# Kernel tuning notes

Measured on AMD Instinct MI355X. Metric: run time of the kernel, lower is better.

Reference implementation:

```python
import jax, jax.numpy as jnp
import numpy as np

L, H, C, V, T_MAX = 12, 12, 768, 50257, 1024
D = C // H
LN_EPS = 1e-5


def layer_norm(x, w, b):
    m = jnp.mean(x, axis=-1, keepdims=True)
    v = jnp.mean(jnp.square(x - m), axis=-1, keepdims=True)
    return (x - m) * jax.lax.rsqrt(v + LN_EPS) * w + b


def setup_inputs() -> dict:
    key = jax.random.key(0)
    ks = jax.random.split(key, 16)
    B, T = 2, 1024
    s = 0.02
    inp = {
        "idx": jax.random.randint(ks[0], (B, T), 0, V),
        "wte": jax.random.normal(ks[1], (V, C), jnp.float32) * s,
        "wpe": jax.random.normal(ks[2], (T_MAX, C), jnp.float32) * s,
        # stacked per-layer params, leading axis = layer
        "ln1_w": jnp.ones((L, C), jnp.float32),
        "ln1_b": jnp.zeros((L, C), jnp.float32),
        "Wq": jax.random.normal(ks[3], (L, C, C), jnp.float32) * s,
        "bq": jnp.zeros((L, C), jnp.float32),
        "Wk": jax.random.normal(ks[4], (L, C, C), jnp.float32) * s,
        "bk": jnp.zeros((L, C), jnp.float32),
        "Wv": jax.random.normal(ks[5], (L, C, C), jnp.float32) * s,
        "bv": jnp.zeros((L, C), jnp.float32),
        "Wo": jax.random.normal(ks[6], (L, C, C), jnp.float32) * (s / np.sqrt(2 * L)),
        "bo": jnp.zeros((L, C), jnp.float32),
        "ln2_w": jnp.ones((L, C), jnp.float32),
        "ln2_b": jnp.zeros((L, C), jnp.float32),
        "Wfc": jax.random.normal(ks[7], (L, C, 4 * C), jnp.float32) * s,
        "bfc": jnp.zeros((L, 4 * C), jnp.float32),
        "Wpr": jax.random.normal(ks[8], (L, 4 * C, C), jnp.float32) * (s / np.sqrt(2 * L)),
        "bpr": jnp.zeros((L, C), jnp.float32),
        "ln_f_w": jnp.ones((C,), jnp.float32),
        "ln_f_b": jnp.zeros((C,), jnp.float32),
        "Wlm": jax.random.normal(ks[9], (C, V), jnp.float32) * s,
    }
    return inp


def _forward(idx, wte, wpe, ln1_w, ln1_b, Wq, bq, Wk, bk, Wv, bv, Wo, bo,
             ln2_w, ln2_b, Wfc, bfc, Wpr, bpr, ln_f_w, ln_f_b, Wlm):
    B, T = idx.shape
    x = wte[idx] + wpe[jnp.arange(T)][None, :, :]  # (B,T,C)
    causal = jnp.tril(jnp.ones((T, T), bool))  # (T,T) causal mask
    scale = 1.0 / np.sqrt(D)
    neg_inf = jnp.finfo(x.dtype).min

    def block(x, p):
        (l1w, l1b, wq, bq_, wk, bk_, wv, bv_, wo, bo_,
         l2w, l2b, wfc, bfc_, wpr, bpr_) = p
        h = layer_norm(x, l1w, l1b)
        q = (h @ wq + bq_).reshape(B, T, H, D)
        k = (h @ wk + bk_).reshape(B, T, H, D)
        v = (h @ wv + bv_).reshape(B, T, H, D)
        scores = jnp.einsum("bqhd,bkhd->bhqk", q, k) * scale
        scores = jnp.where(causal[None, None], scores, neg_inf)
        attn = jax.nn.softmax(scores, axis=-1)
        y = jnp.einsum("bhqk,bkhd->bqhd", attn, v).reshape(B, T, C)
        x = x + y @ wo + bo_
        h2 = layer_norm(x, l2w, l2b)
        x = x + jax.nn.gelu(h2 @ wfc + bfc_, approximate=False) @ wpr + bpr_
        return x, None

    params = (ln1_w, ln1_b, Wq, bq, Wk, bk, Wv, bv, Wo, bo,
              ln2_w, ln2_b, Wfc, bfc, Wpr, bpr)
    x, _ = jax.lax.scan(block, x, params)
    x = layer_norm(x, ln_f_w, ln_f_b)
    logits = x @ Wlm  # (B,T,V)
    return logits


def reference(idx, wte, wpe, ln1_w, ln1_b, Wq, bq, Wk, bk, Wv, bv, Wo, bo,
              ln2_w, ln2_b, Wfc, bfc, Wpr, bpr, ln_f_w, ln_f_b, Wlm):
    return _forward(idx, wte, wpe, ln1_w, ln1_b, Wq, bq, Wk, bk, Wv, bv, Wo, bo,
                    ln2_w, ln2_b, Wfc, bfc, Wpr, bpr, ln_f_w, ln_f_b, Wlm)
```

## Files before the change

### kernel.cpp

```cpp
#include <hip/hip_runtime.h>
#include <math.h>
#include <cstddef>


#define Cdim 768
#define Hn   12
#define Ln   12
#define Tn   1024
#define Bn   2
#define Mrows (Bn * Tn)

typedef unsigned short ushort_t;
typedef __bf16 bf16x8 __attribute__((ext_vector_type(8)));
typedef float  f32x4  __attribute__((ext_vector_type(4)));

__device__ __forceinline__ ushort_t f2bf(float v) {
    union { float f; unsigned int u; } x; x.f = v;
    unsigned int r = x.u + 0x7fffu + ((x.u >> 16) & 1u);
    return (ushort_t)(r >> 16);
}
__device__ __forceinline__ float gelu_f(float v) {
    return 0.5f * v * (1.0f + erff(v * 0.70710678118654752f));
}
__device__ __forceinline__ void gload16(const void* g, void* l) {
    __builtin_amdgcn_global_load_lds(
        (const __attribute__((address_space(1))) unsigned int*)g,
        (__attribute__((address_space(3))) unsigned int*)l, 16, 0, 0);
}

__global__ void embed_k(const int* __restrict__ idx, const float* __restrict__ wte,
                        const float* __restrict__ wpe, float* __restrict__ x) {
    int i = blockIdx.x * 256 + threadIdx.x;
    int c  = i % Cdim;
    int bt = i / Cdim;
    int t  = bt % Tn;
    int tok = idx[bt];
    x[i] = wte[(size_t)tok * Cdim + c] + wpe[(size_t)t * Cdim + c];
}

__global__ __launch_bounds__(256) void ln_k(const float* __restrict__ x,
                                            const float* __restrict__ w,
                                            const float* __restrict__ b,
                                            ushort_t* __restrict__ out) {
    int row = blockIdx.x;
    const float* xr = x + (size_t)row * Cdim;
    int t = threadIdx.x;
    float v0 = xr[t], v1 = xr[t + 256], v2 = xr[t + 512];
    float s = v0 + v1 + v2;
    #pragma unroll
    for (int o = 32; o > 0; o >>= 1) s += __shfl_xor(s, o);
    __shared__ float red[8];
    int wid = t >> 6;
    if ((t & 63) == 0) red[wid] = s;
    __syncthreads();
    float mean = (red[0] + red[1] + red[2] + red[3]) * (1.0f / 768.0f);
    float d0 = v0 - mean, d1 = v1 - mean, d2 = v2 - mean;
    float sq = d0 * d0 + d1 * d1 + d2 * d2;
    #pragma unroll
    for (int o = 32; o > 0; o >>= 1) sq += __shfl_xor(sq, o);
    if ((t & 63) == 0) red[4 + wid] = sq;
    __syncthreads();
    float var = (red[4] + red[5] + red[6] + red[7]) * (1.0f / 768.0f);
    float rstd = rsqrtf(var + 1e-5f);
    ushort_t* orow = out + (size_t)row * Cdim;
    orow[t]       = f2bf(d0 * rstd * w[t]       + b[t]);
    orow[t + 256] = f2bf(d1 * rstd * w[t + 256] + b[t + 256]);
    orow[t + 512] = f2bf(d2 * rstd * w[t + 512] + b[t + 512]);
}

__device__ __forceinline__ void tconv_tile(const float* __restrict__ W,
                                           ushort_t* __restrict__ WT,
                                           int K, int N, int n0, int k0, bool guard) {
    __shared__ float t[32][33];
    int x = threadIdx.x & 31, y = threadIdx.x >> 5;
    #pragma unroll
    for (int j = 0; j < 4; ++j) {
        int kk = k0 + y + j * 8, nn = n0 + x;
        t[y + j * 8][x] = (!guard || nn < N) ? W[(size_t)kk * N + nn] : 0.0f;
    }
    __syncthreads();
    #pragma unroll
    for (int j = 0; j < 4; ++j) {
        int nn = n0 + y + j * 8, kk = k0 + x;
        WT[(size_t)nn * K + kk] = f2bf(t[x][y + j * 8]);
    }
}

__global__ __launch_bounds__(256) void wconv_k(const float* __restrict__ W,
                                               ushort_t* __restrict__ WT,
                                               int K, int N) {
    tconv_tile(W, WT, K, N, blockIdx.x * 32, blockIdx.y * 32, true);
}

__device__ __forceinline__ void conv_body(
    int bid,
    const float* Wq, const float* Wk, const float* Wv, const float* Wo,
    const float* Wfc, const float* Wpr,
    const float* bq, const float* bk, const float* bv,
    ushort_t* wqkvt, ushort_t* wot, ushort_t* wfct, ushort_t* wprt,
    float* bqkv) {
    if (bid < 2304) {
        int z = bid / 576, t = bid % 576;
        const float* W = (z == 0) ? Wq : (z == 1) ? Wk : (z == 2) ? Wv : Wo;
        ushort_t* dst = (z < 3) ? (wqkvt + (size_t)z * 768 * 768) : wot;
        tconv_tile(W, dst, 768, 768, (t % 24) * 32, (t / 24) * 32, false);
    } else if (bid < 4608) {
        int t = bid - 2304;
        tconv_tile(Wfc, wfct, 768, 3072, (t % 96) * 32, (t / 96) * 32, false);
    } else if (bid < 6912) {
        int t = bid - 4608;
        tconv_tile(Wpr, wprt, 3072, 768, (t % 24) * 32, (t / 24) * 32, false);
    } else {
        int i = (bid - 6912) * 256 + threadIdx.x;
        bqkv[i] = (i < 768) ? bq[i] : (i < 1536 ? bk[i - 768] : bv[i - 1536]);
    }
}

__global__ __launch_bounds__(256) void conv_layer_k(
    const float* Wq, const float* Wk, const float* Wv, const float* Wo,
    const float* Wfc, const float* Wpr,
    const float* bq, const float* bk, const float* bv,
    ushort_t* wqkvt, ushort_t* wot, ushort_t* wfct, ushort_t* wprt,
    float* bqkv) {
    conv_body(blockIdx.x, Wq, Wk, Wv, Wo, Wfc, Wpr, bq, bk, bv,
              wqkvt, wot, wfct, wprt, bqkv);
}

__global__ __launch_bounds__(256) void conv_all_k(
    const float* Wq, const float* Wk, const float* Wv, const float* Wo,
    const float* Wfc, const float* Wpr,
    const float* bq, const float* bk, const float* bv,
    ushort_t* wqkvt, ushort_t* wot, ushort_t* wfct, ushort_t* wprt,
    float* bqkv) {
    int l = blockIdx.x / 6921, bid = blockIdx.x % 6921;
    const size_t o2 = (size_t)l * 768 * 768;
    const size_t o4 = (size_t)l * 768 * 3072;
    conv_body(bid,
              Wq + o2, Wk + o2, Wv + o2, Wo + o2, Wfc + o4, Wpr + o4,
              bq + l * 768, bk + l * 768, bv + l * 768,
              wqkvt + (size_t)l * 2304 * 768, wot + o2,
              wfct + o4, wprt + o4, bqkv + l * 2304);
}

template <int BM, int BN, int TH, int WGN,
          bool BIAS, bool GELU_, bool RES, bool OUTBF16, bool XCD, bool QKV>
__global__ __launch_bounds__(TH, 2) void gemm_pipe_k(
    const ushort_t* __restrict__ A,
    const ushort_t* __restrict__ Bt,
    const float* __restrict__ bias,
    const float* __restrict__ res,
    void* __restrict__ Cout,
    ushort_t* __restrict__ kdst,
    ushort_t* __restrict__ vdst,
    int M, int N, int K, int cpx, int mtiles) {
    constexpr int SA = BM * 128;
    constexpr int SB = BN * 128;
    constexpr int WM = BM / 2;
    constexpr int WN = BN / WGN;
    constexpr int FM = WM / 16;
    constexpr int FN = WN / 16;
    constexpr int RJ = TH / 8;
    constexpr int JA = BM / RJ;
    constexpr int JB = BN / RJ;
    constexpr int NL = JA + JB;
    static_assert(NL == 4 || NL == 6 || NL == 8, "vmcnt immediate");
    __shared__ char lds[2 * (SA + SB)];
    char* Abase = lds;
    char* Bbase = lds + 2 * SA;

    const int tid = threadIdx.x;
    const int lane = tid & 63;
    const int w = tid >> 6;
    const int wr = w / WGN, wc = w % WGN;
    int m0, n0;
    if (XCD) {
        int lid = ((int)blockIdx.x & 7) * cpx + ((int)blockIdx.x >> 3);
        m0 = (lid % mtiles) * BM;
        n0 = (lid / mtiles) * BN;
    } else {
        m0 = blockIdx.y * BM;
        n0 = blockIdx.x * BN;
    }

    f32x4 acc[FM][FN] = {};

    const int srowl = tid >> 3;
    const int sslot = (tid & 7) ^ (srowl & 7);
    const ushort_t* Asrc = A  + (size_t)(m0 + srowl) * K + sslot * 8;
    const ushort_t* Bsrc = Bt + (size_t)(n0 + srowl) * K + sslot * 8;

    auto stageall = [&](int d, int kt) {
        const ushort_t* As = Asrc + kt * 64;
        const ushort_t* Bs = Bsrc + kt * 64;
        #pragma unroll
        for (int j = 0; j < JA; ++j)
            gload16(As + (size_t)(j * RJ) * K, Abase + d * SA + tid * 16 + j * (TH * 16));
        #pragma unroll
        for (int j = 0; j < JB; ++j)
            gload16(Bs + (size_t)(j * RJ) * K, Bbase + d * SB + tid * 16 + j * (TH * 16));
    };
    auto readA = [&](int d, int m, int ks) -> bf16x8 {
        int rl = wr * WM + m * 16 + (lane & 15);
        int s  = ks * 4 + (lane >> 4);
        return *(const bf16x8*)(Abase + d * SA + rl * 128 + ((s ^ (rl & 7)) << 4));
    };
    auto readB = [&](int d, int n, int ks) -> bf16x8 {
        int rl = wc * WN + n * 16 + (lane & 15);
        int s  = ks * 4 + (lane >> 4);
        return *(const bf16x8*)(Bbase + d * SB + rl * 128 + ((s ^ (rl & 7)) << 4));
    };

    const int nt = K >> 6;
    stageall(0, 0);
    for (int kt = 0; kt < nt; ++kt) {
        const int d = kt & 1;
        if (kt + 1 < nt) {
            stageall(d ^ 1, kt + 1);
            if constexpr (NL == 8)      asm volatile("s_waitcnt vmcnt(8)" ::: "memory");
            else if constexpr (NL == 6) asm volatile("s_waitcnt vmcnt(6)" ::: "memory");
            else                        asm volatile("s_waitcnt vmcnt(4)" ::: "memory");
        } else {
            asm volatile("s_waitcnt vmcnt(0)" ::: "memory");
        }
        __builtin_amdgcn_s_barrier();
        asm volatile("" ::: "memory");

        bf16x8 bfr[FN][2];
        #pragma unroll
        for (int n = 0; n < FN; ++n) {
            bfr[n][0] = readB(d, n, 0);
            bfr[n][1] = readB(d, n, 1);
        }
        __builtin_amdgcn_s_setprio(1);
        #pragma unroll
        for (int m = 0; m < FM; ++m) {
            bf16x8 a0 = readA(d, m, 0);
            bf16x8 a1 = readA(d, m, 1);
            #pragma unroll
            for (int n = 0; n < FN; ++n) {
                acc[m][n] = __builtin_amdgcn_mfma_f32_16x16x32_bf16(
                    a0, bfr[n][0], acc[m][n], 0, 0, 0);
                acc[m][n] = __builtin_amdgcn_mfma_f32_16x16x32_bf16(
                    a1, bfr[n][1], acc[m][n], 0, 0, 0);
            }
        }
        __builtin_amdgcn_s_setprio(0);
        asm volatile("" ::: "memory");
        __builtin_amdgcn_s_barrier();
    }

    const int r0 = (lane >> 4) * 4, c0 = lane & 15;
    if constexpr (QKV) {
        const int region = n0 / 768;
        #pragma unroll
        for (int m = 0; m < FM; ++m)
            #pragma unroll
            for (int n = 0; n < FN; ++n) {
                int col = n0 + wc * WN + n * 16 + c0;
                int row0 = m0 + wr * WM + m * 16 + r0;
                float vv[4];
                #pragma unroll
                for (int q = 0; q < 4; ++q) vv[q] = acc[m][n][q] + bias[col];
                if (region == 0) {
                    #pragma unroll
                    for (int q = 0; q < 4; ++q)
                        ((ushort_t*)Cout)[(size_t)(row0 + q) * 768 + col] = f2bf(vv[q]);
                } else if (region == 1) {
                    int ck = col - 768, h = ck >> 6, dd = ck & 63;
                    #pragma unroll
                    for (int q = 0; q < 4; ++q) {
                        int row = row0 + q;
                        kdst[(((size_t)(row >> 10) * Hn + h) * Tn + (row & 1023)) * 64 + dd]
                            = f2bf(vv[q]);
                    }
                } else {
                    int cv = col - 1536, h = cv >> 6, dd = cv & 63;
                    int bb = row0 >> 10, tok = row0 & 1023;
                    ushort4 pk;
                    pk.x = f2bf(vv[0]); pk.y = f2bf(vv[1]);
                    pk.z = f2bf(vv[2]); pk.w = f2bf(vv[3]);
                    *(ushort4*)&vdst[(((size_t)bb * Hn + h) * 64 + dd) * Tn + tok] = pk;
                }
            }
        return;
    }
    #pragma unroll
    for (int m = 0; m < FM; ++m)
        #pragma unroll
        for (int n = 0; n < FN; ++n) {
            int col = n0 + wc * WN + n * 16 + c0;
            if (col < N) {
                #pragma unroll
                for (int q = 0; q < 4; ++q) {
                    int row = m0 + wr * WM + m * 16 + r0 + q;
                    float v = acc[m][n][q];
                    if (BIAS) v += bias[col];
                    if (GELU_) v = gelu_f(v);
                    if (RES) v += res[(size_t)row * N + col];
                    if (OUTBF16) ((ushort_t*)Cout)[(size_t)row * N + col] = f2bf(v);
                    else         ((float*)Cout)[(size_t)row * N + col] = v;
                }
            }
        }
}

__global__ __launch_bounds__(256) void attn_mfma_k(
    const ushort_t* __restrict__ qb,
    const ushort_t* __restrict__ kpb,
    const ushort_t* __restrict__ vtb,
    ushort_t* __restrict__ yb) {
    __shared__ ushort_t Ks[64][72];
    __shared__ ushort_t Vt[64][72];
    __shared__ ushort_t Pl[4][16][72];
    const int chunk = (Tn / 64 - 1) - blockIdx.x;
    const int h = blockIdx.y, b = blockIdx.z;
    const int tid = threadIdx.x, lane = tid & 63, w = tid >> 6;
    const int c = lane & 15, g = lane >> 4;
    const int qrow0 = chunk * 64 + w * 16;

    const ushort_t* qp = qb + (size_t)(b * Tn + qrow0 + c) * Cdim + h * 64 + g * 8;
    bf16x8 qa0 = *(const bf16x8*)qp;
    bf16x8 qa1 = *(const bf16x8*)(qp + 32);

    f32x4 accO[4] = {};
    float mrun[4], lrun[4];
    #pragma unroll
    for (int q = 0; q < 4; ++q) { mrun[q] = -1e30f; lrun[q] = 0.0f; }

    const int skey = tid >> 2, sd0 = (tid & 3) * 16;
    const ushort_t* ksrc = kpb + ((size_t)(b * Hn + h) * Tn + skey) * 64 + sd0;
    const int vd = tid >> 2, vseg = tid & 3;
    const ushort_t* vsrc = vtb + ((size_t)(b * Hn + h) * 64 + vd) * Tn + vseg * 16;
    ushort_t* KsW = &Ks[skey][sd0];
    ushort_t* VtW = &Vt[vd][vseg * 16];

    uint4 kr0, kr1, vr0, vr1;
    auto loadt = [&](int kt) {
        const ushort_t* kp = ksrc + (size_t)kt * 64 * 64;
        kr0 = *(const uint4*)kp;
        kr1 = *(const uint4*)(kp + 8);
        const ushort_t* vp = vsrc + kt * 64;
        vr0 = *(const uint4*)vp;
        vr1 = *(const uint4*)(vp + 8);
    };

    const int ntiles = chunk + 1;
    loadt(0);
    for (int kt = 0; kt < ntiles; ++kt) {
        __syncthreads();
        *(uint4*)KsW       = kr0;
        *(uint4*)(KsW + 8) = kr1;
        *(uint4*)VtW       = vr0;
        *(uint4*)(VtW + 8) = vr1;
        __syncthreads();
        if (kt + 1 < ntiles) loadt(kt + 1);

        f32x4 sf[4];
        #pragma unroll
        for (int nk = 0; nk < 4; ++nk) {
            bf16x8 kf0 = *(const bf16x8*)&Ks[nk * 16 + c][g * 8];
            bf16x8 kf1 = *(const bf16x8*)&Ks[nk * 16 + c][g * 8 + 32];
            f32x4 z = {};
            z = __builtin_amdgcn_mfma_f32_16x16x32_bf16(qa0, kf0, z, 0, 0, 0);
            z = __builtin_amdgcn_mfma_f32_16x16x32_bf16(qa1, kf1, z, 0, 0, 0);
            sf[nk] = z;
        }
        float pmax[4] = {-1e30f, -1e30f, -1e30f, -1e30f};
        #pragma unroll
        for (int nk = 0; nk < 4; ++nk) {
            int key = kt * 64 + nk * 16 + c;
            #pragma unroll
            for (int q = 0; q < 4; ++q) {
                float sv = sf[nk][q];
                int row = qrow0 + g * 4 + q;
                sv = (key > row) ? -1e30f : sv;
                sf[nk][q] = sv;
                pmax[q] = fmaxf(pmax[q], sv);
            }
        }
        #pragma unroll
        for (int q = 0; q < 4; ++q)
            #pragma unroll
            for (int off = 1; off < 16; off <<= 1)
                pmax[q] = fmaxf(pmax[q], __shfl_xor(pmax[q], off));
        float corr[4], psum[4];
        #pragma unroll
        for (int q = 0; q < 4; ++q) {
            float mn = fmaxf(mrun[q], pmax[q]);
            corr[q] = __expf((mrun[q] - mn) * 0.125f);
            mrun[q] = mn;
            psum[q] = 0.0f;
        }
        #pragma unroll
        for (int nk = 0; nk < 4; ++nk)
            #pragma unroll
            for (int q = 0; q < 4; ++q) {
                float p = __expf((sf[nk][q] - mrun[q]) * 0.125f);
                psum[q] += p;
                Pl[w][g * 4 + q][nk * 16 + c] = f2bf(p);
            }
        #pragma unroll
        for (int q = 0; q < 4; ++q) {
            #pragma unroll
            for (int off = 1; off < 16; off <<= 1)
                psum[q] += __shfl_xor(psum[q], off);
            lrun[q] = lrun[q] * corr[q] + psum[q];
        }
        #pragma unroll
        for (int ni = 0; ni < 4; ++ni)
            #pragma unroll
            for (int q = 0; q < 4; ++q)
                accO[ni][q] *= corr[q];

        asm volatile("" ::: "memory");
        bf16x8 pa0 = *(const bf16x8*)&Pl[w][c][g * 8];
        bf16x8 pa1 = *(const bf16x8*)&Pl[w][c][g * 8 + 32];
        #pragma unroll
        for (int ni = 0; ni < 4; ++ni) {
            bf16x8 bv0 = *(const bf16x8*)&Vt[ni * 16 + c][g * 8];
            bf16x8 bv1 = *(const bf16x8*)&Vt[ni * 16 + c][g * 8 + 32];
            accO[ni] = __builtin_amdgcn_mfma_f32_16x16x32_bf16(pa0, bv0, accO[ni], 0, 0, 0);
            accO[ni] = __builtin_amdgcn_mfma_f32_16x16x32_bf16(pa1, bv1, accO[ni], 0, 0, 0);
        }
    }

    #pragma unroll
    for (int q = 0; q < 4; ++q) {
        float inv = 1.0f / lrun[q];
        ushort_t* yr = yb + (size_t)(b * Tn + qrow0 + g * 4 + q) * Cdim + h * 64;
        #pragma unroll
        for (int ni = 0; ni < 4; ++ni)
            yr[ni * 16 + c] = f2bf(accO[ni][q] * inv);
    }
}

extern "C" void kernel_launch(void* const* d_in, const int* in_sizes, int n_in,
                              void* d_out, int out_size, void* d_ws, size_t ws_size,
                              hipStream_t stream) {
    const int*   idx  = (const int*)d_in[0];
    const float* wte  = (const float*)d_in[1];
    const float* wpe  = (const float*)d_in[2];
    const float* ln1w = (const float*)d_in[3];
    const float* ln1b = (const float*)d_in[4];
    const float* Wq   = (const float*)d_in[5];
    const float* bq   = (const float*)d_in[6];
    const float* Wk   = (const float*)d_in[7];
    const float* bk   = (const float*)d_in[8];
    const float* Wv   = (const float*)d_in[9];
    const float* bv   = (const float*)d_in[10];
    const float* Wo   = (const float*)d_in[11];
    const float* bo   = (const float*)d_in[12];
    const float* ln2w = (const float*)d_in[13];
    const float* ln2b = (const float*)d_in[14];
    const float* Wfc  = (const float*)d_in[15];
    const float* bfc  = (const float*)d_in[16];
    const float* Wpr  = (const float*)d_in[17];
    const float* bpr  = (const float*)d_in[18];
    const float* lnfw = (const float*)d_in[19];
    const float* lnfb = (const float*)d_in[20];
    const float* Wlm  = (const float*)d_in[21];
    float* out = (float*)d_out;

    const int M = Mrows;
    const int V = out_size / M;
    const int Vpad = ((V + 255) / 256) * 256;

    const size_t SZ_QKV = (size_t)2304 * 768;
    const size_t SZ_O   = (size_t)768 * 768;
    const size_t SZ_FC  = (size_t)3072 * 768;
    const size_t SZ_PR  = (size_t)768 * 3072;
    const size_t SZ_L   = SZ_QKV + SZ_O + SZ_FC + SZ_PR;

    float*    x     = (float*)d_ws;
    float*    bqkvb = x + (size_t)M * Cdim;
    ushort_t* qb    = (ushort_t*)(bqkvb + 12 * 2304);
    ushort_t* kpb   = qb + (size_t)M * Cdim;
    ushort_t* vtb   = kpb + (size_t)Bn * Hn * Tn * 64;
    ushort_t* hb    = vtb + (size_t)Bn * Hn * 64 * Tn;
    ushort_t* yb    = hb + (size_t)M * Cdim;
    ushort_t* mid   = yb + (size_t)M * Cdim;
    ushort_t* wlmt  = mid + (size_t)M * 3072;
    ushort_t* wbase = wlmt + (size_t)Vpad * Cdim;

    const size_t used_common = (size_t)((char*)wbase - (char*)d_ws);
    const bool big = ws_size >= used_common + 12 * SZ_L * sizeof(ushort_t);

    embed_k<<<(M * Cdim) / 256, 256, 0, stream>>>(idx, wte, wpe, x);
    wconv_k<<<dim3(Vpad / 32, 24), 256, 0, stream>>>(Wlm, wlmt, Cdim, V);

    ushort_t* wqkvt0 = wbase;
    ushort_t* wot0   = wqkvt0 + SZ_QKV;
    ushort_t* wfct0  = wot0 + SZ_O;
    ushort_t* wprt0  = wfct0 + SZ_FC;

    if (big) {
        ushort_t* qkvt_all = wbase;
        ushort_t* ot_all   = qkvt_all + 12 * SZ_QKV;
        ushort_t* fct_all  = ot_all + 12 * SZ_O;
        ushort_t* prt_all  = fct_all + 12 * SZ_FC;
        conv_all_k<<<12 * 6921, 256, 0, stream>>>(
            Wq, Wk, Wv, Wo, Wfc, Wpr, bq, bk, bv,
            qkvt_all, ot_all, fct_all, prt_all, bqkvb);
        for (int l = 0; l < Ln; ++l) {
            ushort_t* wqkvt = qkvt_all + (size_t)l * SZ_QKV;
            ushort_t* wot   = ot_all   + (size_t)l * SZ_O;
            ushort_t* wfct  = fct_all  + (size_t)l * SZ_FC;
            ushort_t* wprt  = prt_all  + (size_t)l * SZ_PR;
            float*    bqkv  = bqkvb + l * 2304;
            ln_k<<<M, 256, 0, stream>>>(x, ln1w + l * Cdim, ln1b + l * Cdim, hb);
            gemm_pipe_k<128, 64, 256, 2, true, false, false, true, false, true>
                <<<dim3(36, 16), 256, 0, stream>>>(
                hb, wqkvt, bqkv, nullptr, qb, kpb, vtb, M, 2304, Cdim, 0, 0);
            attn_mfma_k<<<dim3(16, Hn, Bn), 256, 0, stream>>>(qb, kpb, vtb, yb);
            gemm_pipe_k<64, 64, 256, 2, true, false, true, false, false, false>
                <<<dim3(12, 32), 256, 0, stream>>>(
                yb, wot, bo + l * Cdim, x, x, nullptr, nullptr, M, Cdim, Cdim, 0, 0);
            ln_k<<<M, 256, 0, stream>>>(x, ln2w + l * Cdim, ln2b + l * Cdim, hb);
            gemm_pipe_k<128, 64, 256, 2, true, true, false, true, false, false>
                <<<dim3(48, 16), 256, 0, stream>>>(
                hb, wfct, bfc + (size_t)l * 4 * Cdim, nullptr, mid,
                nullptr, nullptr, M, 3072, Cdim, 0, 0);
            gemm_pipe_k<64, 64, 256, 2, true, false, true, false, false, false>
                <<<dim3(12, 32), 256, 0, stream>>>(
                mid, wprt, bpr + l * Cdim, x, x, nullptr, nullptr, M, Cdim, 3072, 0, 0);
        }
    } else {
        for (int l = 0; l < Ln; ++l) {
            const size_t wo2 = (size_t)l * Cdim * Cdim;
            const size_t wo4 = (size_t)l * Cdim * 4 * Cdim;
            conv_layer_k<<<6921, 256, 0, stream>>>(
                Wq + wo2, Wk + wo2, Wv + wo2, Wo + wo2, Wfc + wo4, Wpr + wo4,
                bq + l * Cdim, bk + l * Cdim, bv + l * Cdim,
                wqkvt0, wot0, wfct0, wprt0, bqkvb);
            ln_k<<<M, 256, 0, stream>>>(x, ln1w + l * Cdim, ln1b + l * Cdim, hb);
            gemm_pipe_k<128, 64, 256, 2, true, false, false, true, false, true>
                <<<dim3(36, 16), 256, 0, stream>>>(
                hb, wqkvt0, bqkvb, nullptr, qb, kpb, vtb, M, 2304, Cdim, 0, 0);
            attn_mfma_k<<<dim3(16, Hn, Bn), 256, 0, stream>>>(qb, kpb, vtb, yb);
            gemm_pipe_k<64, 64, 256, 2, true, false, true, false, false, false>
                <<<dim3(12, 32), 256, 0, stream>>>(
                yb, wot0, bo + l * Cdim, x, x, nullptr, nullptr, M, Cdim, Cdim, 0, 0);
            ln_k<<<M, 256, 0, stream>>>(x, ln2w + l * Cdim, ln2b + l * Cdim, hb);
            gemm_pipe_k<128, 64, 256, 2, true, true, false, true, false, false>
                <<<dim3(48, 16), 256, 0, stream>>>(
                hb, wfct0, bfc + (size_t)l * 4 * Cdim, nullptr, mid,
                nullptr, nullptr, M, 3072, Cdim, 0, 0);
            gemm_pipe_k<64, 64, 256, 2, true, false, true, false, false, false>
                <<<dim3(12, 32), 256, 0, stream>>>(
                mid, wprt0, bpr + l * Cdim, x, x, nullptr, nullptr, M, Cdim, 3072, 0, 0);
        }
    }

    ln_k<<<M, 256, 0, stream>>>(x, lnfw, lnfb, hb);
    const int nblk = 16 * (Vpad / 128);
    gemm_pipe_k<128, 128, 256, 2, false, false, false, false, true, false>
        <<<nblk, 256, 0, stream>>>(
        hb, wlmt, nullptr, nullptr, out, nullptr, nullptr, M, V, Cdim, nblk / 8, 16);
}
```

Baseline: 1.785 ms.

## Split-K the N=768 projection GEMMs and fold the reduction into LayerNorm

The attention-output and MLP-projection GEMMs (N=768) now run split-K with two K halves. Each half writes an fp32 partial to its own buffer. The following LayerNorm kernel sums the residual, both partials and the bias, writes the updated residual back, and then normalizes. The aim is to double block count on these under-occupied GEMMs and drop their separate residual/bias epilogue, at the cost of extra fp32 partial-buffer traffic and more loads in LayerNorm.

```diff
diff --git a/kernel.cpp b/kernel.cpp
--- a/kernel.cpp
+++ b/kernel.cpp
@@ -38,14 +38,27 @@
     x[i] = wte[(size_t)tok * Cdim + c] + wpe[(size_t)t * Cdim + c];
 }
 
-__global__ __launch_bounds__(256) void ln_k(const float* __restrict__ x,
+template <bool HASP>
+__global__ __launch_bounds__(256) void ln_k(float* __restrict__ x,
+                                            const float* __restrict__ p0,
+                                            const float* __restrict__ p1,
+                                            const float* __restrict__ pb,
                                             const float* __restrict__ w,
                                             const float* __restrict__ b,
                                             ushort_t* __restrict__ out) {
     int row = blockIdx.x;
-    const float* xr = x + (size_t)row * Cdim;
+    float* xr = x + (size_t)row * Cdim;
     int t = threadIdx.x;
-    float v0 = xr[t], v1 = xr[t + 256], v2 = xr[t + 512];
+    float v0, v1, v2;
+    if (HASP) {
+        size_t base = (size_t)row * Cdim;
+        v0 = xr[t]       + p0[base + t]       + p1[base + t]       + pb[t];
+        v1 = xr[t + 256] + p0[base + t + 256] + p1[base + t + 256] + pb[t + 256];
+        v2 = xr[t + 512] + p0[base + t + 512] + p1[base + t + 512] + pb[t + 512];
+        xr[t] = v0; xr[t + 256] = v1; xr[t + 512] = v2;
+    } else {
+        v0 = xr[t]; v1 = xr[t + 256]; v2 = xr[t + 512];
+    }
     float s = v0 + v1 + v2;
     #pragma unroll
     for (int o = 32; o > 0; o >>= 1) s += __shfl_xor(s, o);
@@ -143,7 +156,8 @@
 }
 
 template <int BM, int BN, int TH, int WGN,
-          bool BIAS, bool GELU_, bool RES, bool OUTBF16, bool XCD, bool QKV>
+          bool BIAS, bool GELU_, bool RES, bool OUTBF16, bool XCD, bool QKV,
+          bool SPLITK>
 __global__ __launch_bounds__(TH, 2) void gemm_pipe_k(
     const ushort_t* __restrict__ A,
     const ushort_t* __restrict__ Bt,
@@ -152,7 +166,7 @@
     void* __restrict__ Cout,
     ushort_t* __restrict__ kdst,
     ushort_t* __restrict__ vdst,
-    int M, int N, int K, int cpx, int mtiles) {
+    int M, int N, int K, int Kloop, int cpx, int mtiles) {
     constexpr int SA = BM * 128;
     constexpr int SB = BN * 128;
     constexpr int WM = BM / 2;
@@ -181,13 +195,15 @@
         m0 = blockIdx.y * BM;
         n0 = blockIdx.x * BN;
     }
+    const int kz = SPLITK ? (int)blockIdx.z : 0;
+    const size_t kzoff = (size_t)kz * Kloop;
 
     f32x4 acc[FM][FN] = {};
 
     const int srowl = tid >> 3;
     const int sslot = (tid & 7) ^ (srowl & 7);
-    const ushort_t* Asrc = A  + (size_t)(m0 + srowl) * K + sslot * 8;
-    const ushort_t* Bsrc = Bt + (size_t)(n0 + srowl) * K + sslot * 8;
+    const ushort_t* Asrc = A  + (size_t)(m0 + srowl) * K + kzoff + sslot * 8;
+    const ushort_t* Bsrc = Bt + (size_t)(n0 + srowl) * K + kzoff + sslot * 8;
 
     auto stageall = [&](int d, int kt) {
         const ushort_t* As = Asrc + kt * 64;
@@ -210,7 +226,7 @@
         return *(const bf16x8*)(Bbase + d * SB + rl * 128 + ((s ^ (rl & 7)) << 4));
     };
 
-    const int nt = K >> 6;
+    const int nt = Kloop >> 6;
     stageall(0, 0);
     for (int kt = 0; kt < nt; ++kt) {
         const int d = kt & 1;
@@ -284,6 +300,21 @@
             }
         return;
     }
+    if constexpr (SPLITK) {
+        float* dst = (float*)Cout + (size_t)kz * M * N;
+        #pragma unroll
+        for (int m = 0; m < FM; ++m)
+            #pragma unroll
+            for (int n = 0; n < FN; ++n) {
+                int col = n0 + wc * WN + n * 16 + c0;
+                #pragma unroll
+                for (int q = 0; q < 4; ++q) {
+                    int row = m0 + wr * WM + m * 16 + r0 + q;
+                    dst[(size_t)row * N + col] = acc[m][n][q];
+                }
+            }
+        return;
+    }
     #pragma unroll
     for (int m = 0; m < FM; ++m)
         #pragma unroll
@@ -473,7 +504,9 @@
 
     float*    x     = (float*)d_ws;
     float*    bqkvb = x + (size_t)M * Cdim;
-    ushort_t* qb    = (ushort_t*)(bqkvb + 12 * 2304);
+    float*    opart = bqkvb + 12 * 2304;
+    float*    ppart = opart + 2 * (size_t)M * Cdim;
+    ushort_t* qb    = (ushort_t*)(ppart + 2 * (size_t)M * Cdim);
     ushort_t* kpb   = qb + (size_t)M * Cdim;
     ushort_t* vtb   = kpb + (size_t)Bn * Hn * Tn * 64;
     ushort_t* hb    = vtb + (size_t)Bn * Hn * 64 * Tn;
@@ -493,67 +526,75 @@
     ushort_t* wfct0  = wot0 + SZ_O;
     ushort_t* wprt0  = wfct0 + SZ_FC;
 
-    if (big) {
-        ushort_t* qkvt_all = wbase;
-        ushort_t* ot_all   = qkvt_all + 12 * SZ_QKV;
-        ushort_t* fct_all  = ot_all + 12 * SZ_O;
-        ushort_t* prt_all  = fct_all + 12 * SZ_FC;
+    ushort_t* qkvt_all = wbase;
+    ushort_t* ot_all   = qkvt_all + 12 * SZ_QKV;
+    ushort_t* fct_all  = ot_all + 12 * SZ_O;
+    ushort_t* prt_all  = fct_all + 12 * SZ_FC;
+
+    if (big)
         conv_all_k<<<12 * 6921, 256, 0, stream>>>(
             Wq, Wk, Wv, Wo, Wfc, Wpr, bq, bk, bv,
             qkvt_all, ot_all, fct_all, prt_all, bqkvb);
-        for (int l = 0; l < Ln; ++l) {
-            ushort_t* wqkvt = qkvt_all + (size_t)l * SZ_QKV;
-            ushort_t* wot   = ot_all   + (size_t)l * SZ_O;
-            ushort_t* wfct  = fct_all  + (size_t)l * SZ_FC;
-            ushort_t* wprt  = prt_all  + (size_t)l * SZ_PR;
-            float*    bqkv  = bqkvb + l * 2304;
-            ln_k<<<M, 256, 0, stream>>>(x, ln1w + l * Cdim, ln1b + l * Cdim, hb);
-            gemm_pipe_k<128, 64, 256, 2, true, false, false, true, false, true>
-                <<<dim3(36, 16), 256, 0, stream>>>(
-                hb, wqkvt, bqkv, nullptr, qb, kpb, vtb, M, 2304, Cdim, 0, 0);
-            attn_mfma_k<<<dim3(16, Hn, Bn), 256, 0, stream>>>(qb, kpb, vtb, yb);
-            gemm_pipe_k<64, 64, 256, 2, true, false, true, false, false, false>
-                <<<dim3(12, 32), 256, 0, stream>>>(
-                yb, wot, bo + l * Cdim, x, x, nullptr, nullptr, M, Cdim, Cdim, 0, 0);
-            ln_k<<<M, 256, 0, stream>>>(x, ln2w + l * Cdim, ln2b + l * Cdim, hb);
-            gemm_pipe_k<128, 64, 256, 2, true, true, false, true, false, false>
-                <<<dim3(48, 16), 256, 0, stream>>>(
-                hb, wfct, bfc + (size_t)l * 4 * Cdim, nullptr, mid,
-                nullptr, nullptr, M, 3072, Cdim, 0, 0);
-            gemm_pipe_k<64, 64, 256, 2, true, false, true, false, false, false>
-                <<<dim3(12, 32), 256, 0, stream>>>(
-                mid, wprt, bpr + l * Cdim, x, x, nullptr, nullptr, M, Cdim, 3072, 0, 0);
-        }
-    } else {
-        for (int l = 0; l < Ln; ++l) {
+
+    for (int l = 0; l < Ln; ++l) {
+        ushort_t *wqkvt, *wot, *wfct, *wprt;
+        float* bqkv;
+        if (big) {
+            wqkvt = qkvt_all + (size_t)l * SZ_QKV;
+            wot   = ot_all   + (size_t)l * SZ_O;
+            wfct  = fct_all  + (size_t)l * SZ_FC;
+            wprt  = prt_all  + (size_t)l * SZ_PR;
+            bqkv  = bqkvb + l * 2304;
+        } else {
             const size_t wo2 = (size_t)l * Cdim * Cdim;
             const size_t wo4 = (size_t)l * Cdim * 4 * Cdim;
             conv_layer_k<<<6921, 256, 0, stream>>>(
                 Wq + wo2, Wk + wo2, Wv + wo2, Wo + wo2, Wfc + wo4, Wpr + wo4,
                 bq + l * Cdim, bk + l * Cdim, bv + l * Cdim,
                 wqkvt0, wot0, wfct0, wprt0, bqkvb);
-            ln_k<<<M, 256, 0, stream>>>(x, ln1w + l * Cdim, ln1b + l * Cdim, hb);
-            gemm_pipe_k<128, 64, 256, 2, true, false, false, true, false, true>
-                <<<dim3(36, 16), 256, 0, stream>>>(
-                hb, wqkvt0, bqkvb, nullptr, qb, kpb, vtb, M, 2304, Cdim, 0, 0);
-            attn_mfma_k<<<dim3(16, Hn, Bn), 256, 0, stream>>>(qb, kpb, vtb, yb);
-            gemm_pipe_k<64, 64, 256, 2, true, false, true, false, false, false>
-                <<<dim3(12, 32), 256, 0, stream>>>(
-                yb, wot0, bo + l * Cdim, x, x, nullptr, nullptr, M, Cdim, Cdim, 0, 0);
-            ln_k<<<M, 256, 0, stream>>>(x, ln2w + l * Cdim, ln2b + l * Cdim, hb);
-            gemm_pipe_k<128, 64, 256, 2, true, true, false, true, false, false>
-                <<<dim3(48, 16), 256, 0, stream>>>(
-                hb, wfct0, bfc + (size_t)l * 4 * Cdim, nullptr, mid,
-                nullptr, nullptr, M, 3072, Cdim, 0, 0);
-            gemm_pipe_k<64, 64, 256, 2, true, false, true, false, false, false>
-                <<<dim3(12, 32), 256, 0, stream>>>(
-                mid, wprt0, bpr + l * Cdim, x, x, nullptr, nullptr, M, Cdim, 3072, 0, 0);
-        }
-    }
-
-    ln_k<<<M, 256, 0, stream>>>(x, lnfw, lnfb, hb);
+            wqkvt = wqkvt0; wot = wot0; wfct = wfct0; wprt = wprt0; bqkv = bqkvb;
+        }
+
+        if (l == 0)
+            ln_k<false><<<M, 256, 0, stream>>>(
+                x, nullptr, nullptr, nullptr, ln1w, ln1b, hb);
+        else
+            ln_k<true><<<M, 256, 0, stream>>>(
+                x, ppart, ppart + (size_t)M * Cdim, bpr + (l - 1) * Cdim,
+                ln1w + l * Cdim, ln1b + l * Cdim, hb);
+
+        gemm_pipe_k<128, 64, 256, 2, true, false, false, true, false, true, false>
+            <<<dim3(36, 16), 256, 0, stream>>>(
+            hb, wqkvt, bqkv, nullptr, qb, kpb, vtb, M, 2304, Cdim, Cdim, 0, 0);
+        attn_mfma_k<<<dim3(16, Hn, Bn), 256, 0, stream>>>(qb, kpb, vtb, yb);
+
+        gemm_pipe_k<64, 64, 256, 2, false, false, false, false, false, false, true>
+            <<<dim3(12, 32, 2), 256, 0, stream>>>(
+            yb, wot, nullptr, nullptr, opart, nullptr, nullptr,
+            M, Cdim, Cdim, Cdim / 2, 0, 0);
+
+        ln_k<true><<<M, 256, 0, stream>>>(
+            x, opart, opart + (size_t)M * Cdim, bo + l * Cdim,
+            ln2w + l * Cdim, ln2b + l * Cdim, hb);
+
+        gemm_pipe_k<128, 64, 256, 2, true, true, false, true, false, false, false>
+            <<<dim3(48, 16), 256, 0, stream>>>(
+            hb, wfct, bfc + (size_t)l * 4 * Cdim, nullptr, mid,
+            nullptr, nullptr, M, 3072, Cdim, Cdim, 0, 0);
+
+        gemm_pipe_k<64, 64, 256, 2, false, false, false, false, false, false, true>
+            <<<dim3(12, 32, 2), 256, 0, stream>>>(
+            mid, wprt, nullptr, nullptr, ppart, nullptr, nullptr,
+            M, Cdim, 3072, 3072 / 2, 0, 0);
+    }
+
+    ln_k<true><<<M, 256, 0, stream>>>(
+        x, ppart, ppart + (size_t)M * Cdim, bpr + (Ln - 1) * Cdim,
+        lnfw, lnfb, hb);
+
     const int nblk = 16 * (Vpad / 128);
-    gemm_pipe_k<128, 128, 256, 2, false, false, false, false, true, false>
+    gemm_pipe_k<128, 128, 256, 2, false, false, false, false, true, false, false>
         <<<nblk, 256, 0, stream>>>(
-        hb, wlmt, nullptr, nullptr, out, nullptr, nullptr, M, V, Cdim, nblk / 8, 16);
-}
+        hb, wlmt, nullptr, nullptr, out, nullptr, nullptr, M, V, Cdim, Cdim,
+        nblk / 8, 16);
+}
```

Measured after the change: 1.800 ms. No clear change (+0.8%).

## Add dedicated 256x256-tile LM-head GEMM kernel with 512 threads and staged pipeline

Applied to the files above, without the earlier changes.

Replaces the generic 128x128 GEMM used for the final vocab projection with a specialized kernel using 256x256 tiles, 8 waves, 128KB of double-buffered LDS with XOR swizzle, and interleaved quarter-tile loads and MFMA phases with priority raising. The larger tile cuts global traffic per FLOP on the largest GEMM in the model. The cost is very high LDS usage, which limits occupancy to one block per CU, and extra tail padding work on V, since Vpad must be a multiple of 256.

```diff
diff --git a/kernel.cpp b/kernel.cpp
--- a/kernel.cpp
+++ b/kernel.cpp
@@ -299,6 +299,118 @@
                     if (RES) v += res[(size_t)row * N + col];
                     if (OUTBF16) ((ushort_t*)Cout)[(size_t)row * N + col] = f2bf(v);
                     else         ((float*)Cout)[(size_t)row * N + col] = v;
+                }
+            }
+        }
+}
+
+__global__ __launch_bounds__(512, 2) void gemm_lm_k(
+    const ushort_t* __restrict__ A,
+    const ushort_t* __restrict__ Bt,
+    float* __restrict__ Cout,
+    int M, int N, int K, int cpx) {
+    __shared__ char lds[131072];
+    char* Abase = lds;
+    char* Bbase = lds + 65536;
+    const int tid = threadIdx.x;
+    const int lane = tid & 63;
+    const int w = tid >> 6;
+    const int wr = w >> 2, wc = w & 3;
+    const int lid = ((int)blockIdx.x & 7) * cpx + ((int)blockIdx.x >> 3);
+    const int m0 = (lid & 7) * 256;
+    const int n0 = (lid >> 3) * 256;
+
+    f32x4 acc[8][4] = {};
+
+    const int srowl = tid >> 3;
+    const int sslot = (tid & 7) ^ (srowl & 7);
+    const ushort_t* Asrc = A  + (size_t)(m0 + srowl) * K + sslot * 8;
+    const ushort_t* Bsrc = Bt + (size_t)(n0 + srowl) * K + sslot * 8;
+    const int ldst = tid * 16;
+
+    auto stage = [&](int d, int ht, int kt) {
+        int h = ht & 1;
+        if (ht < 2) {
+            gload16(Asrc + (size_t)(h * 128) * K + kt * 64,
+                    Abase + d * 32768 + h * 16384 + ldst);
+            gload16(Asrc + (size_t)(h * 128 + 64) * K + kt * 64,
+                    Abase + d * 32768 + h * 16384 + 8192 + ldst);
+        } else {
+            gload16(Bsrc + (size_t)(h * 128) * K + kt * 64,
+                    Bbase + d * 32768 + h * 16384 + ldst);
+            gload16(Bsrc + (size_t)(h * 128 + 64) * K + kt * 64,
+                    Bbase + d * 32768 + h * 16384 + 8192 + ldst);
+        }
+    };
+    auto readA = [&](int d, int m, int ks) -> bf16x8 {
+        int rl = m * 16 + (lane & 15);
+        int s  = ks * 4 + (lane >> 4);
+        return *(const bf16x8*)(Abase + d * 32768 + wr * 16384 + rl * 128 +
+                                ((s ^ (rl & 7)) << 4));
+    };
+    auto readB = [&](int d, int n, int ks) -> bf16x8 {
+        int rl = (wc & 1) * 64 + n * 16 + (lane & 15);
+        int s  = ks * 4 + (lane >> 4);
+        return *(const bf16x8*)(Bbase + d * 32768 + (wc >> 1) * 16384 + rl * 128 +
+                                ((s ^ (rl & 7)) << 4));
+    };
+
+    const int nt = K >> 6;
+    #pragma unroll
+    for (int ht = 0; ht < 4; ++ht) stage(0, ht, 0);
+
+    for (int kt = 0; kt < nt; ++kt) {
+        const int d = kt & 1;
+        bf16x8 bfr[4][2];
+        #pragma unroll
+        for (int p = 0; p < 4; ++p) {
+            if (kt + 1 < nt) stage(d ^ 1, p, kt + 1);
+            if (p == 0) {
+                if (kt + 1 < nt) asm volatile("s_waitcnt vmcnt(2)" ::: "memory");
+                else             asm volatile("s_waitcnt vmcnt(0)" ::: "memory");
+            }
+            __builtin_amdgcn_s_barrier();
+            asm volatile("" ::: "memory");
+            if (p == 0) {
+                #pragma unroll
+                for (int n = 0; n < 4; ++n)
+                    #pragma unroll
+                    for (int ks = 0; ks < 2; ++ks) bfr[n][ks] = readB(d, n, ks);
+            }
+            bf16x8 af[2][2];
+            #pragma unroll
+            for (int mm = 0; mm < 2; ++mm)
+                #pragma unroll
+                for (int ks = 0; ks < 2; ++ks) af[mm][ks] = readA(d, p * 2 + mm, ks);
+            asm volatile("s_waitcnt lgkmcnt(0)" ::: "memory");
+            __builtin_amdgcn_sched_barrier(0);
+            __builtin_amdgcn_s_setprio(1);
+            #pragma unroll
+            for (int mm = 0; mm < 2; ++mm)
+                #pragma unroll
+                for (int n = 0; n < 4; ++n)
+                    #pragma unroll
+                    for (int ks = 0; ks < 2; ++ks)
+                        acc[p * 2 + mm][n] = __builtin_amdgcn_mfma_f32_16x16x32_bf16(
+                            af[mm][ks], bfr[n][ks], acc[p * 2 + mm][n], 0, 0, 0);
+            __builtin_amdgcn_s_setprio(0);
+            __builtin_amdgcn_sched_barrier(0);
+            asm volatile("" ::: "memory");
+            __builtin_amdgcn_s_barrier();
+        }
+    }
+
+    const int r0 = (lane >> 4) * 4, c0 = lane & 15;
+    #pragma unroll
+    for (int m = 0; m < 8; ++m)
+        #pragma unroll
+        for (int n = 0; n < 4; ++n) {
+            int col = n0 + wc * 64 + n * 16 + c0;
+            if (col < N) {
+                #pragma unroll
+                for (int q = 0; q < 4; ++q) {
+                    int row = m0 + wr * 128 + m * 16 + r0 + q;
+                    Cout[(size_t)row * N + col] = acc[m][n][q];
                 }
             }
         }
@@ -552,8 +664,6 @@
     }
 
     ln_k<<<M, 256, 0, stream>>>(x, lnfw, lnfb, hb);
-    const int nblk = 16 * (Vpad / 128);
-    gemm_pipe_k<128, 128, 256, 2, false, false, false, false, true, false>
-        <<<nblk, 256, 0, stream>>>(
-        hb, wlmt, nullptr, nullptr, out, nullptr, nullptr, M, V, Cdim, nblk / 8, 16);
-}
+    const int nblk = (Vpad / 256) * 8;
+    gemm_lm_k<<<nblk, 512, 0, stream>>>(hb, wlmt, out, M, V, Cdim, nblk / 8);
+}
```

Result: no change. 1.791 ms (+0.4%).
